# Optimization experiments

Measured on AMD Instinct MI355X. Metric: run time of the kernel, lower is better.

The kernel has to match this reference:

```python
import jax, jax.numpy as jnp
import numpy as np

B, T, D, H, L = 32, 129, 96, 64, 1
SLOPE = 0.2  # LeakyReLU slope


def setup_inputs() -> dict:
    key = jax.random.key(0)
    ks = jax.random.split(key, 6)
    x = jax.random.normal(ks[0], (B, T, D), dtype=jnp.float32)
    alphas = jax.random.normal(ks[1], (D, D), dtype=jnp.float32)
    # Per-latent-dim MLP gs[i]: Linear(D+1+i -> H) -> LeakyReLU -> Linear(H -> 1),
    # padded to a common input width 2D. mask[i, d] = 1 iff d < D+1+i (real columns).
    mask = (np.arange(2 * D)[None, :] <= (D + np.arange(D))[:, None]).astype(np.float32)
    W1 = jax.random.normal(ks[2], (D, 2 * D, H), dtype=jnp.float32) * (1.0 / np.sqrt(2 * D))
    W1 = W1 * mask[:, :, None]
    b1 = jax.random.normal(ks[3], (D, H), dtype=jnp.float32) * 0.01
    W2 = jax.random.normal(ks[4], (D, H), dtype=jnp.float32) * (1.0 / np.sqrt(H))
    b2 = jax.random.normal(ks[5], (D,), dtype=jnp.float32) * 0.01
    return {"x": x, "alphas": alphas, "W1": W1, "b1": b1, "W2": W2, "b2": b2}


def reference(x, alphas, W1, b1, W2, b2):
    Bb, Tt, Dd = x.shape
    N = Bb * (Tt - L)
    # unfold(dim=1, size=L+1, step=1) with L=1: window t is (x_t, x_{t+1})
    yy = x[:, : Tt - L].reshape(N, Dd)          # past lag  -> [N, D]
    xx = x[:, L:].reshape(N, Dd)                # current   -> [N, D]
    idx = jnp.arange(Dd)
    # coefficient on xx[:, k] for output dim i: alphas[i,k] if k<i, 1 if k==i, 0 else
    M = alphas * (idx[None, :] < idx[:, None]).astype(x.dtype) + jnp.eye(Dd, dtype=x.dtype)
    tail = xx[:, None, :] * M[None, :, :]                       # [N, D, D]
    yyb = jnp.broadcast_to(yy[:, None, :], (N, Dd, Dd))         # [N, D, D]
    inp = jnp.concatenate([yyb, tail], axis=-1)                 # [N, D, 2D] padded inputs
    # Forward through all D per-dim MLPs at once
    h = jnp.einsum('nid,idh->nih', inp, W1) + b1                # [N, D, H]
    a = jnp.where(h > 0, h, SLOPE * h)
    residuals = jnp.einsum('nih,ih->ni', a, W2) + b2            # [N, D]
    # Analytic Jacobian of each scalar MLP: J = W2 @ diag(act') @ W1
    dact = jnp.where(h > 0, jnp.asarray(1.0, x.dtype), jnp.asarray(SLOPE, x.dtype))
    pdd = jnp.einsum('nih,ih,idh->nid', dact, W2, W1)           # [N, D, 2D]
    last_col = Dd + idx                                          # position of xx[:, i] input
    last = pdd[:, idx, last_col]                                 # [N, D] d residual_i / d xx_i
    sum_log_abs_det = jnp.sum(jnp.log(jnp.abs(last)), axis=-1).reshape(Bb, Tt - L).sum(axis=1)
    # hist_jac: Jacobian w.r.t. all inputs except the last real one (zero-padded to 2D)
    hist_jac = pdd.at[:, idx, last_col].set(0.0)                 # [N, D, 2D]
    return residuals.reshape(Bb, Tt - L, Dd), sum_log_abs_det, hist_jac
```

## Files before the change

### kernel.cpp

```cpp
#include <hip/hip_runtime.h>
#include <cmath>


#define TILE_N 64
#define NTHR   512

__global__ void zero_slad_kernel(float* __restrict__ p) {
    if (threadIdx.x < 32) p[threadIdx.x] = 0.0f;
}

__global__ __launch_bounds__(NTHR, 2)
void fused_flow_kernel(const float* __restrict__ x,
                       const float* __restrict__ alphas,
                       const float* __restrict__ W1,
                       const float* __restrict__ b1,
                       const float* __restrict__ W2,
                       const float* __restrict__ b2,
                       float* __restrict__ out_resid,
                       float* __restrict__ out_slad,
                       float* __restrict__ out_hist)
{
    const int i   = blockIdx.y;
    const int n0  = blockIdx.x * TILE_N;
    const int tid = threadIdx.x;

    __shared__ float sA[13056];
    __shared__ float sW1[12288];
    __shared__ float sG[64*68];
    __shared__ float sM[96];
    __shared__ float sW2v[64];
    __shared__ float sB1v[64];
    __shared__ float sRes[64*33];
    __shared__ float sLog[64];

    if (tid < 96) {
        float v = 0.0f;
        if (tid < i) v = alphas[i*96 + tid];
        else if (tid == i) v = 1.0f;
        sM[tid] = v;
    } else if (tid < 160) {
        sW2v[tid-96] = W2[i*64 + (tid-96)];
    } else if (tid < 224) {
        sB1v[tid-160] = b1[i*64 + (tid-160)];
    }
    __syncthreads();

    {
        const float4* src = reinterpret_cast<const float4*>(W1 + (size_t)i * 12288);
        float4* dst = reinterpret_cast<float4*>(sW1);
        #pragma unroll
        for (int j = 0; j < 6; ++j) dst[tid + j*NTHR] = src[tid + j*NTHR];
    }

    {
        const int bb = n0 >> 7;
        const int t0 = n0 & 127;
        const float* xbase = x + (size_t)(bb*129 + t0) * 96;
        #pragma unroll
        for (int j = 0; j < 6; ++j) {
            int idx = tid + j*NTHR;
            int r = idx / 48;
            int c = idx - r*48;
            float4 v = *reinterpret_cast<const float4*>(xbase + r*96 + c*4);
            int d0 = c*4;
            if (d0 >= 96) {
                v.x *= sM[d0-96]; v.y *= sM[d0-95]; v.z *= sM[d0-94]; v.w *= sM[d0-93];
            }
            sA[(d0+0)*68 + r] = v.x;
            sA[(d0+1)*68 + r] = v.y;
            sA[(d0+2)*68 + r] = v.z;
            sA[(d0+3)*68 + r] = v.w;
        }
    }
    __syncthreads();

    const int tm = tid & 15;
    const int th = tid >> 4;
    const int m0 = tm * 4;
    const int h0 = th * 2;

    float acc1[4][2];
    #pragma unroll
    for (int a = 0; a < 4; ++a)
        #pragma unroll
        for (int q = 0; q < 2; ++q) acc1[a][q] = 0.0f;

    const int Kd = 97 + i;
    #pragma unroll 4
    for (int k = 0; k < Kd; ++k) {
        const float4 av = *reinterpret_cast<const float4*>(&sA[k*68 + m0]);
        const float2 bv = *reinterpret_cast<const float2*>(&sW1[(k<<6) + h0]);
        const float am[4] = {av.x, av.y, av.z, av.w};
        const float bh[2] = {bv.x, bv.y};
        #pragma unroll
        for (int a = 0; a < 4; ++a)
            #pragma unroll
            for (int q = 0; q < 2; ++q)
                acc1[a][q] = __builtin_fmaf(am[a], bh[q], acc1[a][q]);
    }

    {
        float resp[4] = {0.f, 0.f, 0.f, 0.f};
        #pragma unroll
        for (int q = 0; q < 2; ++q) {
            const float b1q = sB1v[h0+q];
            const float w2q = sW2v[h0+q];
            #pragma unroll
            for (int a = 0; a < 4; ++a) {
                const float hv = acc1[a][q] + b1q;
                const bool pos = hv > 0.0f;
                resp[a] += (pos ? hv : 0.2f*hv) * w2q;
                sG[(h0+q)*68 + (m0+a)] = (pos ? 1.0f : 0.2f) * w2q;
            }
        }
        #pragma unroll
        for (int a = 0; a < 4; ++a) sRes[(m0+a)*33 + th] = resp[a];
    }
    __syncthreads();

    #pragma unroll
    for (int j = 0; j < 6; ++j) {
        int idx = tid + j*NTHR;
        int hh = idx & 63;
        int kc = idx >> 6;
        float4 v;
        v.x = sW1[(kc*4+0)*64 + hh];
        v.y = sW1[(kc*4+1)*64 + hh];
        v.z = sW1[(kc*4+2)*64 + hh];
        v.w = sW1[(kc*4+3)*64 + hh];
        *reinterpret_cast<float4*>(&sA[hh*196 + kc*4]) = v;
    }
    __syncthreads();

    const int td  = tid & 15;
    const int tm2 = tid >> 4;
    const int d0  = td * 12;
    const int p0  = tm2 * 2;

    float acc2[2][12];
    #pragma unroll
    for (int a = 0; a < 2; ++a)
        #pragma unroll
        for (int q = 0; q < 12; ++q) acc2[a][q] = 0.0f;

    if (d0 <= 96 + i) {
        #pragma unroll 2
        for (int k = 0; k < 64; ++k) {
            const float2 av  = *reinterpret_cast<const float2*>(&sG[k*68 + p0]);
            const float4 b0v = *reinterpret_cast<const float4*>(&sA[k*196 + d0 + 0]);
            const float4 b1v = *reinterpret_cast<const float4*>(&sA[k*196 + d0 + 4]);
            const float4 b2v = *reinterpret_cast<const float4*>(&sA[k*196 + d0 + 8]);
            const float am[2]  = {av.x, av.y};
            const float bd[12] = {b0v.x, b0v.y, b0v.z, b0v.w,
                                  b1v.x, b1v.y, b1v.z, b1v.w,
                                  b2v.x, b2v.y, b2v.z, b2v.w};
            #pragma unroll
            for (int a = 0; a < 2; ++a)
                #pragma unroll
                for (int q = 0; q < 12; ++q)
                    acc2[a][q] = __builtin_fmaf(am[a], bd[q], acc2[a][q]);
        }
    }

    {
        const int lc  = 96 + i;
        const int tdl = lc / 12;
        if (td == tdl) {
            const int qlc = lc - tdl*12;
            #pragma unroll
            for (int q = 0; q < 12; ++q) {
                if (q == qlc) {
                    #pragma unroll
                    for (int a = 0; a < 2; ++a) {
                        sLog[p0+a] = logf(fabsf(acc2[a][q]));
                        acc2[a][q] = 0.0f;
                    }
                }
            }
        }
    }

    #pragma unroll
    for (int a = 0; a < 2; ++a) {
        float* row = out_hist + ((size_t)(n0 + p0 + a)*96 + i)*192 + d0;
        *reinterpret_cast<float4*>(row + 0) = make_float4(acc2[a][0], acc2[a][1], acc2[a][2],  acc2[a][3]);
        *reinterpret_cast<float4*>(row + 4) = make_float4(acc2[a][4], acc2[a][5], acc2[a][6],  acc2[a][7]);
        *reinterpret_cast<float4*>(row + 8) = make_float4(acc2[a][8], acc2[a][9], acc2[a][10], acc2[a][11]);
    }
    __syncthreads();

    if (tid < 64) {
        float s = b2[i];
        #pragma unroll
        for (int j = 0; j < 32; ++j) s += sRes[tid*33 + j];
        out_resid[(size_t)(n0 + tid)*96 + i] = s;

        float lp = sLog[tid];
        #pragma unroll
        for (int off = 32; off > 0; off >>= 1) lp += __shfl_down(lp, off);
        if (tid == 0) atomicAdd(&out_slad[n0 >> 7], lp);
    }
}

extern "C" void kernel_launch(void* const* d_in, const int* in_sizes, int n_in,
                              void* d_out, int out_size, void* d_ws, size_t ws_size,
                              hipStream_t stream) {
    const float* x      = (const float*)d_in[0];
    const float* alphas = (const float*)d_in[1];
    const float* W1     = (const float*)d_in[2];
    const float* b1     = (const float*)d_in[3];
    const float* W2     = (const float*)d_in[4];
    const float* b2     = (const float*)d_in[5];

    float* out       = (float*)d_out;
    float* out_resid = out;
    float* out_slad  = out + 4096*96;
    float* out_hist  = out + 4096*96 + 32;

    zero_slad_kernel<<<1, 64, 0, stream>>>(out_slad);

    dim3 grid(4096 / TILE_N, 96);
    fused_flow_kernel<<<grid, NTHR, 0, stream>>>(x, alphas, W1, b1, W2, b2,
                                                 out_resid, out_slad, out_hist);
}
```

Measured before the change: 669.7 us.

## Drop shared W1 staging, read W1 from global/L2 to raise occupancy

Removes the 48 KB shared-memory copy of W1. The first GEMM now reads W1 directly from global memory through the cache, and the transposed W1 tile is built straight from global. This cuts LDS use per block so more blocks can be resident, and the launch bound is raised to 4 blocks per CU. It also changes the thread-to-row mapping of the x load so each thread takes a fixed row. The cost is uncached-latency global loads inside the inner k loop of the first GEMM and register pressure under the tighter launch bound.

```diff
diff --git a/kernel.cpp b/kernel.cpp
--- a/kernel.cpp
+++ b/kernel.cpp
@@ -9,7 +9,7 @@
     if (threadIdx.x < 32) p[threadIdx.x] = 0.0f;
 }
 
-__global__ __launch_bounds__(NTHR, 2)
+__global__ __launch_bounds__(NTHR, 4)
 void fused_flow_kernel(const float* __restrict__ x,
                        const float* __restrict__ alphas,
                        const float* __restrict__ W1,
@@ -25,13 +25,14 @@
     const int tid = threadIdx.x;
 
     __shared__ float sA[13056];
-    __shared__ float sW1[12288];
     __shared__ float sG[64*68];
     __shared__ float sM[96];
     __shared__ float sW2v[64];
     __shared__ float sB1v[64];
     __shared__ float sRes[64*33];
     __shared__ float sLog[64];
+
+    const float* __restrict__ W1i = W1 + (size_t)i * 12288;
 
     if (tid < 96) {
         float v = 0.0f;
@@ -46,23 +47,16 @@
     __syncthreads();
 
     {
-        const float4* src = reinterpret_cast<const float4*>(W1 + (size_t)i * 12288);
-        float4* dst = reinterpret_cast<float4*>(sW1);
-        #pragma unroll
-        for (int j = 0; j < 6; ++j) dst[tid + j*NTHR] = src[tid + j*NTHR];
-    }
-
-    {
         const int bb = n0 >> 7;
         const int t0 = n0 & 127;
         const float* xbase = x + (size_t)(bb*129 + t0) * 96;
+        const int r  = tid & 63;
+        const int c0 = tid >> 6;
         #pragma unroll
         for (int j = 0; j < 6; ++j) {
-            int idx = tid + j*NTHR;
-            int r = idx / 48;
-            int c = idx - r*48;
+            const int c = c0 + 8*j;
             float4 v = *reinterpret_cast<const float4*>(xbase + r*96 + c*4);
-            int d0 = c*4;
+            const int d0 = c*4;
             if (d0 >= 96) {
                 v.x *= sM[d0-96]; v.y *= sM[d0-95]; v.z *= sM[d0-94]; v.w *= sM[d0-93];
             }
@@ -86,10 +80,11 @@
         for (int q = 0; q < 2; ++q) acc1[a][q] = 0.0f;
 
     const int Kd = 97 + i;
+    const float* __restrict__ bptr = W1i + h0;
     #pragma unroll 4
     for (int k = 0; k < Kd; ++k) {
         const float4 av = *reinterpret_cast<const float4*>(&sA[k*68 + m0]);
-        const float2 bv = *reinterpret_cast<const float2*>(&sW1[(k<<6) + h0]);
+        const float2 bv = *reinterpret_cast<const float2*>(bptr + (k<<6));
         const float am[4] = {av.x, av.y, av.z, av.w};
         const float bh[2] = {bv.x, bv.y};
         #pragma unroll
@@ -118,17 +113,19 @@
     }
     __syncthreads();
 
-    #pragma unroll
-    for (int j = 0; j < 6; ++j) {
-        int idx = tid + j*NTHR;
-        int hh = idx & 63;
-        int kc = idx >> 6;
-        float4 v;
-        v.x = sW1[(kc*4+0)*64 + hh];
-        v.y = sW1[(kc*4+1)*64 + hh];
-        v.z = sW1[(kc*4+2)*64 + hh];
-        v.w = sW1[(kc*4+3)*64 + hh];
-        *reinterpret_cast<float4*>(&sA[hh*196 + kc*4]) = v;
+    {
+        const int hh  = tid & 63;
+        const int kc0 = tid >> 6;
+        #pragma unroll
+        for (int j = 0; j < 6; ++j) {
+            const int kc = kc0 + 8*j;
+            float4 v;
+            v.x = W1i[(kc*4+0)*64 + hh];
+            v.y = W1i[(kc*4+1)*64 + hh];
+            v.z = W1i[(kc*4+2)*64 + hh];
+            v.w = W1i[(kc*4+3)*64 + hh];
+            *reinterpret_cast<float4*>(&sA[hh*196 + kc*4]) = v;
+        }
     }
     __syncthreads();
 
```

New measurement: 651.9 us. 1.03x faster.
